# Optimization experiments

Measured on AMD Instinct MI355X. Metric: run time of the kernel, lower is better.

Reference implementation:

```python
import math
import jax, jax.numpy as jnp
import numpy as np

B, T, M, S, D, H = 16, 512, 8, 32, 256, 4
HD = D // H


def setup_inputs() -> dict:
    key = jax.random.key(0)
    ks = jax.random.split(key, 16)
    w = 1.0 / math.sqrt(D)
    return {
        'q_temporal': jax.random.normal(ks[0], (B, T, M, D), jnp.float32),
        'q_static': jax.random.normal(ks[1], (B, S, D), jnp.float32),
        'k_temporal': jax.random.normal(ks[2], (B, T, M, D), jnp.float32),
        'v_temporal': jax.random.normal(ks[3], (B, T, M, D), jnp.float32),
        'k_static': jax.random.normal(ks[4], (B, S, D), jnp.float32),
        'v_static': jax.random.normal(ks[5], (B, S, D), jnp.float32),
        'q_w': jax.random.normal(ks[6], (D, D), jnp.float32) * w,
        'q_b': jax.random.normal(ks[7], (D,), jnp.float32) * w,
        'k_w': jax.random.normal(ks[8], (D, D), jnp.float32) * w,
        'k_b': jax.random.normal(ks[9], (D,), jnp.float32) * w,
        'v_w': jax.random.normal(ks[10], (D, D), jnp.float32) * w,
        'v_b': jax.random.normal(ks[11], (D,), jnp.float32) * w,
        'o_w': jax.random.normal(ks[12], (D, D), jnp.float32) * w,
        'o_b': jax.random.normal(ks[13], (D,), jnp.float32) * w,
        'mask_temporal': jax.random.randint(ks[14], (B, T, M), 0, 2).astype(jnp.int32),
        'mask_fcst': jax.random.randint(ks[15], (B, T, M), 0, 2).astype(jnp.int32),
        'mask_static': jnp.ones((B, S), jnp.int32),
    }


def _lin(x, w, b):
    # torch.nn.Linear: y = x @ W^T + b
    return x @ w.T + b


def reference(q_temporal, q_static, k_temporal, v_temporal, k_static, v_static,
              q_w, q_b, k_w, k_b, v_w, v_b, o_w, o_b,
              mask_temporal, mask_fcst, mask_static):
    scale = 1.0 / math.sqrt(HD)

    def heads5(x):  # [B,T,M,D] -> [B,H,T,M,HD]
        return x.reshape(B, T, M, H, HD).transpose(0, 3, 1, 2, 4)

    def heads3(x):  # [B,S,D] -> [B,H,S,HD]
        return x.reshape(B, -1, H, HD).transpose(0, 2, 1, 3)

    Qt = heads5(_lin(q_temporal, q_w, q_b))
    Kt = heads5(_lin(k_temporal, k_w, k_b))
    Vt = heads5(_lin(v_temporal, v_w, v_b))
    Qs = heads3(_lin(q_static, q_w, q_b))
    Ks = heads3(_lin(k_static, k_w, k_b))
    Vs = heads3(_lin(v_static, v_w, v_b))

    # additive masks: 0 where valid (==1), -inf where padded
    mt = jnp.where(mask_temporal == 1, 0.0, -jnp.inf).astype(Qt.dtype)  # [B,T,M]
    ms = jnp.where(mask_static == 1, 0.0, -jnp.inf).astype(Qt.dtype)    # [B,S]

    # ---- temporal query branch ----
    # temp_temp: per-timestep modality-vs-modality attention, column key mask
    Qt_Kt = jnp.einsum('bhtmd,bhtnd->bhtmn', Qt, Kt) * scale + mt[:, None, :, None, :]
    # temp_static: temporal queries vs static keys
    Qt_Ks = jnp.einsum('bhtmd,bhsd->bhtms', Qt, Ks) * scale + ms[:, None, None, None, :]
    tw = jax.nn.softmax(jnp.concatenate([Qt_Kt, Qt_Ks], axis=-1), axis=-1)  # [B,H,T,M,M+S]
    QKV_t = (jnp.einsum('bhtmn,bhtnd->bhtmd', tw[..., :M], Vt)
             + jnp.einsum('bhtms,bhsd->bhtmd', tw[..., M:], Vs))
    out_t = _lin(QKV_t.transpose(0, 2, 3, 1, 4).reshape(B, T, M, D), o_w, o_b)

    # ---- static query branch ----
    Ktf = Kt.reshape(B, H, T * M, HD)  # flatten (T,M) key axis
    Vtf = Vt.reshape(B, H, T * M, HD)
    Qs_Kt = jnp.einsum('bhqd,bhkd->bhqk', Qs, Ktf) * scale + mt.reshape(B, 1, 1, T * M)
    Qs_Ks = jnp.einsum('bhqd,bhsd->bhqs', Qs, Ks) * scale + ms[:, None, None, :]
    sw = jax.nn.softmax(jnp.concatenate([Qs_Kt, Qs_Ks], axis=-1), axis=-1)  # [B,H,S,T*M+S]
    QKV_s = (jnp.einsum('bhqk,bhkd->bhqd', sw[..., :T * M], Vtf)
             + jnp.einsum('bhqs,bhsd->bhqd', sw[..., T * M:], Vs))
    out_s = _lin(QKV_s.transpose(0, 2, 1, 3).reshape(B, S, D), o_w, o_b)

    return (out_t, out_s, tw, sw)
```

## Files before the change

### kernel.cpp

```cpp
#include <hip/hip_runtime.h>

#define B_   16
#define T_   512
#define M_   8
#define S_   32
#define D_   256
#define H_   4
#define HD_  64
#define TM_  4096
#define NKT  40
#define NKS  4128

typedef unsigned short u16;
typedef __attribute__((ext_vector_type(8))) short bf16x8;
typedef __attribute__((ext_vector_type(4))) float f32x4;

__device__ __forceinline__ u16 f2b(float f) {
    union { float f; unsigned u; } v; v.f = f;
    unsigned r = v.u + 0x7FFF + ((v.u >> 16) & 1);
    return (u16)(r >> 16);
}
__device__ __forceinline__ float blo(unsigned u) {
    union { unsigned i; float f; } v; v.i = u << 16; return v.f;
}
__device__ __forceinline__ float bhi(unsigned u) {
    union { unsigned i; float f; } v; v.i = u & 0xFFFF0000u; return v.f;
}
__device__ __forceinline__ float b2f(u16 u) {
    union { unsigned i; float f; } v; v.i = ((unsigned)u) << 16; return v.f;
}
__device__ __forceinline__ unsigned pack2(float lo, float hi) {
    return (unsigned)f2b(lo) | ((unsigned)f2b(hi) << 16);
}
__device__ __forceinline__ uint4 cvt8(float4 a, float4 b) {
    uint4 r;
    r.x = pack2(a.x, a.y); r.y = pack2(a.z, a.w);
    r.z = pack2(b.x, b.y); r.w = pack2(b.z, b.w);
    return r;
}

#define GLL16(g, l) __builtin_amdgcn_global_load_lds( \
    (const __attribute__((address_space(1))) void*)(g), \
    (__attribute__((address_space(3))) void*)(l), 16, 0, 0)

__global__ __launch_bounds__(256) void k_cvt_w(const float* __restrict__ W0,
                                               const float* __restrict__ W1,
                                               const float* __restrict__ W2,
                                               u16* __restrict__ dst)
{
    const int sel = blockIdx.y;
    const float* W = sel == 0 ? W0 : sel == 1 ? W1 : W2;
    u16* d = dst + sel * 65536;
    const int i0 = (blockIdx.x * 256 + threadIdx.x) * 8;
    const float4 a = *(const float4*)(W + i0);
    const float4 b = *(const float4*)(W + i0 + 4);
    *(uint4*)(d + i0) = cvt8(a, b);
}

template<int XBF, int OUTF32>
__device__ __forceinline__ void gemm_body(const void* __restrict__ Xv,
                                          const u16* __restrict__ Wb,
                                          const float* __restrict__ bias,
                                          void* __restrict__ Yv,
                                          int bx, u16* smem)
{
    const int tid = threadIdx.x;
    const size_t r0 = (size_t)bx * 128;
    const int wave = tid >> 6, lane = tid & 63;
    const int c = lane & 15, g = lane >> 4;
    const int swzk = g ^ ((c >> 1) & 3);
    const int swzl = (lane & 3) ^ ((lane >> 3) & 3);
    u16* sA = smem;
    u16* sB = smem + 10240;
    const int ar = tid >> 1, ah = tid & 1;

    f32x4 acc[8][4];
#pragma unroll
    for (int i = 0; i < 8; ++i)
#pragma unroll
        for (int j = 0; j < 4; ++j) acc[i][j] = (f32x4){0, 0, 0, 0};

    float4 fa[2][4];
    uint4  ua[2][2];

#define LOAD_A(k0, s)                                                           \
    if (XBF) {                                                                  \
        const u16* gA = (const u16*)Xv + (r0 + ar) * 256 + (k0) + ah * 16;      \
        ua[s][0] = *(const uint4*)gA; ua[s][1] = *(const uint4*)(gA + 8);       \
    } else {                                                                    \
        const float* gA = (const float*)Xv + (r0 + ar) * 256 + (k0) + ah * 16;  \
        fa[s][0] = *(const float4*)gA;       fa[s][1] = *(const float4*)(gA + 4); \
        fa[s][2] = *(const float4*)(gA + 8); fa[s][3] = *(const float4*)(gA + 12); \
    }
#define WRITE_A(bi, s)                                                          \
    {   u16* d = sA + (bi) * 5120 + ar * 40 + ah * 16;                          \
        if (XBF) { *(uint4*)d = ua[s][0]; *(uint4*)(d + 8) = ua[s][1]; }        \
        else { *(uint4*)d = cvt8(fa[s][0], fa[s][1]);                           \
               *(uint4*)(d + 8) = cvt8(fa[s][2], fa[s][3]); }                   \
    }
#define STAGE_B(k0, bi)                                                         \
    _Pragma("unroll")                                                           \
    for (int i = 0; i < 4; ++i) {                                               \
        const int row = i * 64 + wave * 16 + (lane >> 2);                       \
        GLL16(Wb + (size_t)row * 256 + (k0) + swzl * 8,                         \
              sB + (bi) * 8192 + (i * 256 + wave * 64) * 8);                    \
    }

    {
        LOAD_A(0, 0)
        WRITE_A(0, 0)
        LOAD_A(32, 0)
        STAGE_B(0, 0)
    }

#pragma unroll
    for (int k = 0; k < 8; ++k) {
        const int cur = k & 1;
        __syncthreads();
        if (k < 6) LOAD_A((k + 2) * 32, (k + 1) & 1)
        if (k < 7) STAGE_B((k + 1) * 32, cur ^ 1)
        bf16x8 a[8], b[4];
#pragma unroll
        for (int f = 0; f < 8; ++f)
            a[f] = *(const bf16x8*)(sA + cur * 5120 + (f * 16 + c) * 40 + g * 8);
#pragma unroll
        for (int f = 0; f < 4; ++f)
            b[f] = *(const bf16x8*)(sB + cur * 8192 + (wave * 64 + f * 16 + c) * 32 + swzk * 8);
#pragma unroll
        for (int rf = 0; rf < 8; ++rf)
#pragma unroll
            for (int cf = 0; cf < 4; ++cf)
                acc[rf][cf] = __builtin_amdgcn_mfma_f32_16x16x32_bf16(
                    a[rf], b[cf], acc[rf][cf], 0, 0, 0);
        if (k < 7) WRITE_A(cur ^ 1, k & 1)
    }
#undef LOAD_A
#undef WRITE_A
#undef STAGE_B

    const int orow = g * 4, ocol = c;
    if (OUTF32) {
#pragma unroll
        for (int cf = 0; cf < 4; ++cf) {
            const int col = wave * 64 + cf * 16 + ocol;
            const float bv = bias[col];
#pragma unroll
            for (int rf = 0; rf < 8; ++rf)
#pragma unroll
                for (int r = 0; r < 4; ++r)
                    ((float*)Yv)[(r0 + rf * 16 + orow + r) * 256 + col] =
                        acc[rf][cf][r] + bv;
        }
    } else {
#pragma unroll
        for (int hh = 0; hh < 2; ++hh) {
            __syncthreads();
#pragma unroll
            for (int cf = 0; cf < 4; ++cf) {
                const int col = wave * 64 + cf * 16 + ocol;
                const float bv = bias[col];
#pragma unroll
                for (int rf4 = 0; rf4 < 4; ++rf4)
#pragma unroll
                    for (int r = 0; r < 4; ++r)
                        smem[(rf4 * 16 + orow + r) * 264 + col] =
                            f2b(acc[hh * 4 + rf4][cf][r] + bv);
            }
            __syncthreads();
#pragma unroll
            for (int i = 0; i < 8; ++i) {
                const int s = i * 256 + tid;
                const int row = s >> 5, seg = s & 31;
                *(uint4*)((u16*)Yv + (r0 + hh * 64 + row) * 256 + seg * 8) =
                    *(const uint4*)(smem + row * 264 + seg * 8);
            }
        }
    }
}

template<int XBF, int OUTF32>
__global__ __launch_bounds__(256, 2) void k_gemm_m(const void* __restrict__ Xv,
                                                   const u16* __restrict__ Wb,
                                                   const float* __restrict__ bias,
                                                   void* __restrict__ Yv)
{
    __shared__ __align__(16) u16 smem[26624];
    gemm_body<XBF, OUTF32>(Xv, Wb, bias, Yv, blockIdx.x, smem);
}

__global__ __launch_bounds__(256, 2) void k_gemm_qkv(
    const float* __restrict__ X0, const float* __restrict__ X1, const float* __restrict__ X2,
    const u16* __restrict__ Wb,
    const float* __restrict__ b0, const float* __restrict__ b1, const float* __restrict__ b2,
    u16* __restrict__ Y0, u16* __restrict__ Y1, u16* __restrict__ Y2)
{
    __shared__ __align__(16) u16 smem[26624];
    const int sel = blockIdx.y;
    const float* X = sel == 0 ? X0 : sel == 1 ? X1 : X2;
    const float* bb = sel == 0 ? b0 : sel == 1 ? b1 : b2;
    u16* Y = sel == 0 ? Y0 : sel == 1 ? Y1 : Y2;
    gemm_body<0, 0>(X, Wb + sel * 65536, bb, Y, blockIdx.x, smem);
}

__global__ __launch_bounds__(256) void k_attn_t(
    const u16* __restrict__ Qt, const u16* __restrict__ Kt, const u16* __restrict__ Vt,
    const u16* __restrict__ Ks, const u16* __restrict__ Vs,
    const int* __restrict__ maskT, const int* __restrict__ maskS,
    float* __restrict__ tw, u16* __restrict__ qkvt)
{
    const int tp = blockIdx.x, b = blockIdx.y;
    const int t0 = tp * 2;
    __shared__ __align__(16) u16 sQ [4 * 2 * 16 * 32];
    __shared__ __align__(16) u16 sKT[4 * 2 * 16 * 32];
    __shared__ __align__(16) u16 sKS[4 * 2 * 32 * 32];
    __shared__ __align__(16) u16 sVT[4 * 64 * 72];
    __shared__ __align__(16) u16 sP [4 * 16 * 72];
    __shared__ int smT[2][8];
    __shared__ int smS[32];
    const int tid = threadIdx.x;

#pragma unroll
    for (int i = 0; i < 2; ++i) {
        const int fl = tid + i * 256;
        const int r = fl >> 5, c32 = fl & 31;
        const int h = c32 >> 3, ks = (c32 >> 2) & 1, seg = c32 & 3;
        const size_t src = (((size_t)b * T_ + t0 + (r >> 3)) * 8 + (r & 7)) * 256 + c32 * 8;
        const int dst = h * 1024 + ks * 512 + r * 32 + seg * 8;
        *(uint4*)(sQ  + dst) = *(const uint4*)(Qt + src);
        *(uint4*)(sKT + dst) = *(const uint4*)(Kt + src);
    }
#pragma unroll
    for (int i = 0; i < 4; ++i) {
        const int fl = tid + i * 256;
        const int r = fl >> 5, c32 = fl & 31;
        const int h = c32 >> 3, ks = (c32 >> 2) & 1, seg = c32 & 3;
        *(uint4*)(sKS + h * 2048 + ks * 1024 + r * 32 + seg * 8) =
            *(const uint4*)(Ks + ((size_t)b * S_ + r) * 256 + c32 * 8);
    }
    {
        const int key = tid & 63, dg = tid >> 6;
        const u16* vrow = nullptr;
        if (key < 16)      vrow = Vt + (((size_t)b * T_ + t0 + (key >> 3)) * 8 + (key & 7)) * 256;
        else if (key < 48) vrow = Vs + ((size_t)b * S_ + (key - 16)) * 256;
#pragma unroll
        for (int i = 0; i < 8; ++i) {
            const int dseg = dg * 8 + i;
            uint4 v = {0, 0, 0, 0};
            if (vrow) v = *(const uint4*)(vrow + dseg * 8);
            const int h = dseg >> 3, dl0 = (dseg & 7) * 8;
            const u16* pv = (const u16*)&v;
#pragma unroll
            for (int j = 0; j < 8; ++j)
                sVT[h * 4608 + (dl0 + j) * 72 + key] = pv[j];
        }
    }
    if (tid < 16) smT[tid >> 3][tid & 7] =
        maskT[((size_t)b * T_ + t0 + (tid >> 3)) * 8 + (tid & 7)];
    if (tid < 32) smS[tid] = maskS[b * S_ + tid];
    __syncthreads();

    const int h = tid >> 6, lane = tid & 63;
    const int c = lane & 15, g = lane >> 4, th = g >> 1;

    f32x4 at = {0,0,0,0}, as0 = {0,0,0,0}, as1 = {0,0,0,0};
#pragma unroll
    for (int ks = 0; ks < 2; ++ks) {
        bf16x8 aq = *(const bf16x8*)(sQ  + h * 1024 + ks * 512 + c * 32 + g * 8);
        bf16x8 bt = *(const bf16x8*)(sKT + h * 1024 + ks * 512 + c * 32 + g * 8);
        bf16x8 b0 = *(const bf16x8*)(sKS + h * 2048 + ks * 1024 + c * 32 + g * 8);
        bf16x8 b1 = *(const bf16x8*)(sKS + h * 2048 + ks * 1024 + 512 + c * 32 + g * 8);
        at  = __builtin_amdgcn_mfma_f32_16x16x32_bf16(aq, bt, at, 0, 0, 0);
        as0 = __builtin_amdgcn_mfma_f32_16x16x32_bf16(aq, b0, as0, 0, 0, 0);
        as1 = __builtin_amdgcn_mfma_f32_16x16x32_bf16(aq, b1, as1, 0, 0, 0);
    }

    const int vt = ((c >> 3) == th) ? smT[th][c & 7] : 0;
    const int v0 = smS[c], v1 = smS[16 + c];
    float st[4], s0[4], s1[4], mx[4];
#pragma unroll
    for (int r = 0; r < 4; ++r) {
        st[r] = vt ? at[r]  * 0.125f : -1e30f;
        s0[r] = v0 ? as0[r] * 0.125f : -1e30f;
        s1[r] = v1 ? as1[r] * 0.125f : -1e30f;
        mx[r] = fmaxf(fmaxf(st[r], s0[r]), s1[r]);
    }
#pragma unroll
    for (int o = 1; o < 16; o <<= 1)
#pragma unroll
        for (int r = 0; r < 4; ++r) mx[r] = fmaxf(mx[r], __shfl_xor(mx[r], o));
    float pt[4], p0[4], p1[4], sum[4];
#pragma unroll
    for (int r = 0; r < 4; ++r) {
        pt[r] = __expf(st[r] - mx[r]);
        p0[r] = __expf(s0[r] - mx[r]);
        p1[r] = __expf(s1[r] - mx[r]);
        sum[r] = pt[r] + p0[r] + p1[r];
    }
#pragma unroll
    for (int o = 1; o < 16; o <<= 1)
#pragma unroll
        for (int r = 0; r < 4; ++r) sum[r] += __shfl_xor(sum[r], o);
#pragma unroll
    for (int r = 0; r < 4; ++r) {
        const float inv = 1.0f / sum[r];
        pt[r] *= inv; p0[r] *= inv; p1[r] *= inv;
    }

#pragma unroll
    for (int r = 0; r < 4; ++r) {
        const int row = g * 4 + r;
        const int tt = t0 + (row >> 3), m = row & 7;
        float* twp = tw + ((((size_t)b * H_ + h) * T_ + tt) * 8 + m) * NKT;
        if ((c >> 3) == th) twp[c & 7] = pt[r];
        twp[8 + c]  = p0[r];
        twp[24 + c] = p1[r];
        u16* sp = sP + h * 1152 + row * 72;
        sp[c]      = f2b(pt[r]);
        sp[16 + c] = f2b(p0[r]);
        sp[32 + c] = f2b(p1[r]);
        sp[48 + c] = 0;
    }

    f32x4 o4[4] = {{0,0,0,0}, {0,0,0,0}, {0,0,0,0}, {0,0,0,0}};
#pragma unroll
    for (int ks = 0; ks < 2; ++ks) {
        bf16x8 pa = *(const bf16x8*)(sP + h * 1152 + c * 72 + ks * 32 + g * 8);
#pragma unroll
        for (int dt = 0; dt < 4; ++dt) {
            bf16x8 pb = *(const bf16x8*)(sVT + h * 4608 + (dt * 16 + c) * 72 + ks * 32 + g * 8);
            o4[dt] = __builtin_amdgcn_mfma_f32_16x16x32_bf16(pa, pb, o4[dt], 0, 0, 0);
        }
    }
#pragma unroll
    for (int dt = 0; dt < 4; ++dt)
#pragma unroll
        for (int r = 0; r < 4; ++r) {
            const int row = g * 4 + r;
            const int tt = t0 + (row >> 3), m = row & 7;
            qkvt[(((size_t)b * T_ + tt) * 8 + m) * 256 + h * 64 + dt * 16 + c] = f2b(o4[dt][r]);
        }
}

__global__ __launch_bounds__(256) void k_attn_s_scores(
    const u16* __restrict__ Qs, const u16* __restrict__ Kt, const u16* __restrict__ Ks,
    const int* __restrict__ maskT, const int* __restrict__ maskS,
    float* __restrict__ raw)
{
    const int ch = blockIdx.x, h = blockIdx.y, b = blockIdx.z;
    const int nk = (ch < 32) ? 128 : 32;
    const int k0 = ch * 128;
    __shared__ __align__(16) u16 sQ[2 * 32 * 32];
    __shared__ __align__(16) u16 sK[2 * 128 * 32];
    __shared__ int sM[128];
    const int tid = threadIdx.x;

    {   const int q = tid >> 3, c8 = tid & 7;
        const int ks = c8 >> 2, seg = c8 & 3;
        *(uint4*)(sQ + ks * 1024 + q * 32 + seg * 8) =
            *(const uint4*)(Qs + ((size_t)b * S_ + q) * 256 + h * 64 + c8 * 8);
    }
#pragma unroll
    for (int i = 0; i < 4; ++i) {
        const int fl = tid + i * 256;
        const int key = fl >> 3, c8 = fl & 7;
        const int ks = c8 >> 2, seg = c8 & 3;
        if (key < nk) {
            const u16* src = (ch < 32)
                ? (Kt + ((size_t)b * TM_ + k0 + key) * 256 + h * 64 + c8 * 8)
                : (Ks + ((size_t)b * S_  +      key) * 256 + h * 64 + c8 * 8);
            *(uint4*)(sK + ks * 4096 + key * 32 + seg * 8) = *(const uint4*)src;
        }
    }
    if (tid < nk) sM[tid] = (ch < 32) ? maskT[(size_t)b * TM_ + k0 + tid]
                                      : maskS[b * S_ + tid];
    __syncthreads();

    const int w = tid >> 6, lane = tid & 63;
    if (w * 32 >= nk) return;
    const int c = lane & 15, g = lane >> 4;

    f32x4 acc[2][2] = {{{0,0,0,0}, {0,0,0,0}}, {{0,0,0,0}, {0,0,0,0}}};
#pragma unroll
    for (int ks = 0; ks < 2; ++ks) {
        bf16x8 a0 = *(const bf16x8*)(sQ + ks * 1024 +        c * 32 + g * 8);
        bf16x8 a1 = *(const bf16x8*)(sQ + ks * 1024 + 512 +  c * 32 + g * 8);
        bf16x8 b0 = *(const bf16x8*)(sK + ks * 4096 + (w * 32 +      c) * 32 + g * 8);
        bf16x8 b1 = *(const bf16x8*)(sK + ks * 4096 + (w * 32 + 16 + c) * 32 + g * 8);
        acc[0][0] = __builtin_amdgcn_mfma_f32_16x16x32_bf16(a0, b0, acc[0][0], 0, 0, 0);
        acc[0][1] = __builtin_amdgcn_mfma_f32_16x16x32_bf16(a0, b1, acc[0][1], 0, 0, 0);
        acc[1][0] = __builtin_amdgcn_mfma_f32_16x16x32_bf16(a1, b0, acc[1][0], 0, 0, 0);
        acc[1][1] = __builtin_amdgcn_mfma_f32_16x16x32_bf16(a1, b1, acc[1][1], 0, 0, 0);
    }
#pragma unroll
    for (int rt = 0; rt < 2; ++rt)
#pragma unroll
        for (int ct = 0; ct < 2; ++ct) {
            const int kl = w * 32 + ct * 16 + c;
            const float madd = sM[kl] ? 0.f : -1e30f;
#pragma unroll
            for (int r = 0; r < 4; ++r) {
                const int q = rt * 16 + g * 4 + r;
                raw[(((size_t)b * H_ + h) * S_ + q) * NKS + k0 + kl] =
                    acc[rt][ct][r] * 0.125f + madd;
            }
        }
}

__global__ __launch_bounds__(256) void k_attn_s_softmax(
    const float* __restrict__ raw, float* __restrict__ sw)
{
    const int q = blockIdx.x, h = blockIdx.y, b = blockIdx.z;
    __shared__ float sRow[NKS];
    __shared__ float red[8];
    const int tid = threadIdx.x;
    const size_t base = (((size_t)b * H_ + h) * S_ + q) * NKS;

    float mx = -1e30f;
    for (int i = tid; i < NKS; i += 256) {
        const float v = raw[base + i];
        sRow[i] = v;
        mx = fmaxf(mx, v);
    }
    for (int o = 32; o; o >>= 1) mx = fmaxf(mx, __shfl_xor(mx, o));
    if ((tid & 63) == 0) red[tid >> 6] = mx;
    __syncthreads();
    mx = fmaxf(fmaxf(red[0], red[1]), fmaxf(red[2], red[3]));

    float sum = 0.f;
    for (int i = tid; i < NKS; i += 256) {
        const float e = __expf(sRow[i] - mx);
        sRow[i] = e;
        sum += e;
    }
    for (int o = 32; o; o >>= 1) sum += __shfl_xor(sum, o);
    if ((tid & 63) == 0) red[4 + (tid >> 6)] = sum;
    __syncthreads();
    sum = (red[4] + red[5]) + (red[6] + red[7]);
    const float inv = 1.0f / sum;

    for (int i = tid; i < NKS; i += 256)
        sw[base + i] = sRow[i] * inv;
}

__global__ __launch_bounds__(256) void k_attn_s_pv_part(
    const float* __restrict__ w, const u16* __restrict__ Vt, const u16* __restrict__ Vs,
    float* __restrict__ part)
{
    const int ch = blockIdx.x, h = blockIdx.y, b = blockIdx.z;
    const int nk = (ch < 32) ? 128 : 32;
    const int k0 = ch * 128;
    __shared__ float sW[32][132];
    __shared__ __align__(16) u16 sV[128 * 64];
    const int tid = threadIdx.x;

#pragma unroll
    for (int i = 0; i < 4; ++i) {
        const int fl = tid + i * 256;
        const int q = fl >> 5, k4 = fl & 31;
        if (k4 * 4 < nk)
            *(float4*)&sW[q][k4 * 4] =
                *(const float4*)(w + (((size_t)b * H_ + h) * S_ + q) * NKS + k0 + k4 * 4);
    }
#pragma unroll
    for (int i = 0; i < 4; ++i) {
        const int fl = tid + i * 256;
        const int key = fl >> 3, pp = fl & 7;
        if (key < nk) {
            const u16* src = (ch < 32)
                ? (Vt + ((size_t)b * TM_ + k0 + key) * D_ + h * HD_ + pp * 8)
                : (Vs + ((size_t)b * S_  +      key) * D_ + h * HD_ + pp * 8);
            ((uint4*)sV)[fl] = *(const uint4*)src;
        }
    }
    __syncthreads();

    const int d = tid & 63, qg = tid >> 6;
    float acc[8] = {0,0,0,0,0,0,0,0};
    for (int kk = 0; kk < nk; kk += 4) {
        const float v0 = b2f(sV[(kk + 0) * 64 + d]);
        const float v1 = b2f(sV[(kk + 1) * 64 + d]);
        const float v2 = b2f(sV[(kk + 2) * 64 + d]);
        const float v3 = b2f(sV[(kk + 3) * 64 + d]);
#pragma unroll
        for (int j = 0; j < 8; ++j) {
            const float4 wv = *(const float4*)&sW[qg * 8 + j][kk];
            acc[j] += wv.x * v0 + wv.y * v1 + wv.z * v2 + wv.w * v3;
        }
    }

    float* pb = part + (((size_t)ch * B_ + b) * H_ + h) * 2048;
#pragma unroll
    for (int j = 0; j < 8; ++j)
        pb[(qg * 8 + j) * 64 + d] = acc[j];
}

__global__ __launch_bounds__(256) void k_attn_s_pv_red(
    const float* __restrict__ part, u16* __restrict__ qkvs)
{
    const int h = blockIdx.x, b = blockIdx.y;
    const int tid = threadIdx.x;
    for (int i = tid; i < 2048; i += 256) {
        float s = 0.f;
#pragma unroll
        for (int c = 0; c < 33; ++c)
            s += part[(((size_t)c * B_ + b) * H_ + h) * 2048 + i];
        const int q = i >> 6, d = i & 63;
        qkvs[((size_t)b * S_ + q) * D_ + h * HD_ + d] = f2b(s);
    }
}

extern "C" void kernel_launch(void* const* d_in, const int* in_sizes, int n_in,
                              void* d_out, int out_size, void* d_ws, size_t ws_size,
                              hipStream_t stream)
{
    const float* q_t = (const float*)d_in[0];
    const float* q_s = (const float*)d_in[1];
    const float* k_t = (const float*)d_in[2];
    const float* v_t = (const float*)d_in[3];
    const float* k_s = (const float*)d_in[4];
    const float* v_s = (const float*)d_in[5];
    const float* q_w = (const float*)d_in[6];
    const float* q_b = (const float*)d_in[7];
    const float* k_w = (const float*)d_in[8];
    const float* k_b = (const float*)d_in[9];
    const float* v_w = (const float*)d_in[10];
    const float* v_b = (const float*)d_in[11];
    const float* o_w = (const float*)d_in[12];
    const float* o_b = (const float*)d_in[13];
    const int* maskT = (const int*)d_in[14];
    const int* maskS = (const int*)d_in[16];
    float* out = (float*)d_out;

    char* ws = (char*)d_ws;
    u16*   Kt   = (u16*)(ws + 0);
    u16*   Vt   = (u16*)(ws + 33554432);
    u16*   QKVt = (u16*)(ws + 67108864);
    float* part = (float*)(ws + 67108864);
    u16*   Wqkv = (u16*)(ws + 67108864);
    u16*   Qs   = (u16*)(ws + 100663296);
    u16*   Ks   = (u16*)(ws + 100925440);
    u16*   Vs   = (u16*)(ws + 101187584);
    u16*   QKVs = (u16*)(ws + 101449728);
    u16*   Qt   = (u16*)(ws + 101711872);
    float* raw  = (float*)(ws + 101711872);
    u16*   Wo   = (u16*)(ws + 101711872);
    if (ws_size < 135528448) return;

    float* out_t = out;
    float* out_s = out + 16777216;
    float* tw    = out + 16908288;
    float* sw    = out + 27394048;

    const dim3 blk(256);
    k_cvt_w<<<dim3(32, 3), blk, 0, stream>>>(q_w, k_w, v_w, Wqkv);

    k_gemm_qkv<<<dim3(512, 3), blk, 0, stream>>>(q_t, k_t, v_t, Wqkv,
                                                 q_b, k_b, v_b, Qt, Kt, Vt);
    k_gemm_qkv<<<dim3(4, 3),   blk, 0, stream>>>(q_s, k_s, v_s, Wqkv,
                                                 q_b, k_b, v_b, Qs, Ks, Vs);

    k_attn_t<<<dim3(256, 16), blk, 0, stream>>>(Qt, Kt, Vt, Ks, Vs, maskT, maskS, tw, QKVt);

    k_cvt_w<<<dim3(32, 1), blk, 0, stream>>>(o_w, o_w, o_w, Wo);
    k_gemm_m<1,1><<<dim3(512), blk, 0, stream>>>(QKVt, Wo, o_b, out_t);

    k_attn_s_scores<<<dim3(33, 4, 16), blk, 0, stream>>>(Qs, Kt, Ks, maskT, maskS, raw);
    k_attn_s_softmax<<<dim3(32, 4, 16), blk, 0, stream>>>(raw, sw);
    k_cvt_w<<<dim3(32, 1), blk, 0, stream>>>(o_w, o_w, o_w, Wo);
    k_attn_s_pv_part<<<dim3(33, 4, 16), blk, 0, stream>>>(sw, Vt, Vs, part);
    k_attn_s_pv_red<<<dim3(4, 16), blk, 0, stream>>>(part, QKVs);

    k_gemm_m<1,1><<<dim3(4),   blk, 0, stream>>>(QKVs, Wo, o_b, out_s);
}
```

Baseline: 267.6 us.

## Rework projection GEMM to 64-row tiles with whole-K A panel preloaded in LDS

Replaces the 128-row tiled GEMM, whose A tile was double-buffered through registers, with a 64-row kernel. That kernel loads the full 64x256 A panel into LDS once (converting fp32 to bf16) and pipelines only the weight tiles. This removes the per-step register staging of A and halves the accumulator count, which should improve occupancy and double the number of blocks. In exchange it puts a large serialized A load up front and reloads the weights twice as often. All four projection GEMM launches are unified into one templated kernel.

```diff
diff --git a/kernel.cpp b/kernel.cpp
--- a/kernel.cpp
+++ b/kernel.cpp
@@ -58,84 +58,82 @@
 }
 
 template<int XBF, int OUTF32>
-__device__ __forceinline__ void gemm_body(const void* __restrict__ Xv,
-                                          const u16* __restrict__ Wb,
-                                          const float* __restrict__ bias,
-                                          void* __restrict__ Yv,
-                                          int bx, u16* smem)
-{
+__global__ __launch_bounds__(256, 2) void k_gemm_db(
+    const void* __restrict__ X0, const void* __restrict__ X1, const void* __restrict__ X2,
+    const u16* __restrict__ Wb, int wstride,
+    const float* __restrict__ b0, const float* __restrict__ b1, const float* __restrict__ b2,
+    void* __restrict__ Y0, void* __restrict__ Y1, void* __restrict__ Y2)
+{
+    __shared__ __align__(16) u16 sA[20480];
+    __shared__ __align__(16) u16 sB[16384];
+    const int sel = blockIdx.y;
+    const void*  Xv   = sel == 0 ? X0 : sel == 1 ? X1 : X2;
+    const float* bias = sel == 0 ? b0 : sel == 1 ? b1 : b2;
+    void*        Yv   = sel == 0 ? Y0 : sel == 1 ? Y1 : Y2;
+    const u16* W = Wb + sel * wstride;
     const int tid = threadIdx.x;
-    const size_t r0 = (size_t)bx * 128;
+    const size_t r0 = (size_t)blockIdx.x * 64;
     const int wave = tid >> 6, lane = tid & 63;
     const int c = lane & 15, g = lane >> 4;
     const int swzk = g ^ ((c >> 1) & 3);
     const int swzl = (lane & 3) ^ ((lane >> 3) & 3);
-    u16* sA = smem;
-    u16* sB = smem + 10240;
-    const int ar = tid >> 1, ah = tid & 1;
-
-    f32x4 acc[8][4];
-#pragma unroll
-    for (int i = 0; i < 8; ++i)
-#pragma unroll
-        for (int j = 0; j < 4; ++j) acc[i][j] = (f32x4){0, 0, 0, 0};
-
-    float4 fa[2][4];
-    uint4  ua[2][2];
-
-#define LOAD_A(k0, s)                                                           \
-    if (XBF) {                                                                  \
-        const u16* gA = (const u16*)Xv + (r0 + ar) * 256 + (k0) + ah * 16;      \
-        ua[s][0] = *(const uint4*)gA; ua[s][1] = *(const uint4*)(gA + 8);       \
-    } else {                                                                    \
-        const float* gA = (const float*)Xv + (r0 + ar) * 256 + (k0) + ah * 16;  \
-        fa[s][0] = *(const float4*)gA;       fa[s][1] = *(const float4*)(gA + 4); \
-        fa[s][2] = *(const float4*)(gA + 8); fa[s][3] = *(const float4*)(gA + 12); \
-    }
-#define WRITE_A(bi, s)                                                          \
-    {   u16* d = sA + (bi) * 5120 + ar * 40 + ah * 16;                          \
-        if (XBF) { *(uint4*)d = ua[s][0]; *(uint4*)(d + 8) = ua[s][1]; }        \
-        else { *(uint4*)d = cvt8(fa[s][0], fa[s][1]);                           \
-               *(uint4*)(d + 8) = cvt8(fa[s][2], fa[s][3]); }                   \
-    }
+
 #define STAGE_B(k0, bi)                                                         \
     _Pragma("unroll")                                                           \
     for (int i = 0; i < 4; ++i) {                                               \
         const int row = i * 64 + wave * 16 + (lane >> 2);                       \
-        GLL16(Wb + (size_t)row * 256 + (k0) + swzl * 8,                         \
+        GLL16(W + (size_t)row * 256 + (k0) + swzl * 8,                          \
               sB + (bi) * 8192 + (i * 256 + wave * 64) * 8);                    \
     }
 
-    {
-        LOAD_A(0, 0)
-        WRITE_A(0, 0)
-        LOAD_A(32, 0)
-        STAGE_B(0, 0)
-    }
+    STAGE_B(0, 0)
+
+    if (XBF) {
+#pragma unroll
+        for (int j = 0; j < 8; ++j) {
+            const int row = j * 8 + wave * 2 + (lane >> 5);
+            const uint4 v = *(const uint4*)((const u16*)Xv + (r0 + row) * 256
+                                            + (lane & 31) * 8);
+            *(uint4*)(sA + ((lane & 31) >> 2) * 2560 + row * 40 + (lane & 3) * 8) = v;
+        }
+    } else {
+#pragma unroll
+        for (int j = 0; j < 16; ++j) {
+            const int row = j * 4 + wave;
+            const float4 v = *(const float4*)((const float*)Xv + (r0 + row) * 256
+                                              + lane * 4);
+            uint2 p; p.x = pack2(v.x, v.y); p.y = pack2(v.z, v.w);
+            *(uint2*)(sA + (lane >> 3) * 2560 + row * 40 + (lane & 7) * 4) = p;
+        }
+    }
+    __syncthreads();
+
+    f32x4 acc[4][4];
+#pragma unroll
+    for (int i = 0; i < 4; ++i)
+#pragma unroll
+        for (int j = 0; j < 4; ++j) acc[i][j] = (f32x4){0, 0, 0, 0};
 
 #pragma unroll
     for (int k = 0; k < 8; ++k) {
         const int cur = k & 1;
-        __syncthreads();
-        if (k < 6) LOAD_A((k + 2) * 32, (k + 1) & 1)
-        if (k < 7) STAGE_B((k + 1) * 32, cur ^ 1)
-        bf16x8 a[8], b[4];
-#pragma unroll
-        for (int f = 0; f < 8; ++f)
-            a[f] = *(const bf16x8*)(sA + cur * 5120 + (f * 16 + c) * 40 + g * 8);
+        if (k < 7) { STAGE_B((k + 1) * 32, cur ^ 1) }
+        bf16x8 a[4], b[4];
 #pragma unroll
         for (int f = 0; f < 4; ++f)
-            b[f] = *(const bf16x8*)(sB + cur * 8192 + (wave * 64 + f * 16 + c) * 32 + swzk * 8);
-#pragma unroll
-        for (int rf = 0; rf < 8; ++rf)
+            a[f] = *(const bf16x8*)(sA + k * 2560 + (f * 16 + c) * 40 + g * 8);
+#pragma unroll
+        for (int f = 0; f < 4; ++f)
+            b[f] = *(const bf16x8*)(sB + cur * 8192
+                                    + (wave * 64 + f * 16 + c) * 32 + swzk * 8);
+#pragma unroll
+        for (int rf = 0; rf < 4; ++rf)
 #pragma unroll
             for (int cf = 0; cf < 4; ++cf)
                 acc[rf][cf] = __builtin_amdgcn_mfma_f32_16x16x32_bf16(
                     a[rf], b[cf], acc[rf][cf], 0, 0, 0);
-        if (k < 7) WRITE_A(cur ^ 1, k & 1)
-    }
-#undef LOAD_A
-#undef WRITE_A
+        if (k < 7) __syncthreads();
+    }
 #undef STAGE_B
 
     const int orow = g * 4, ocol = c;
@@ -145,61 +143,33 @@
             const int col = wave * 64 + cf * 16 + ocol;
             const float bv = bias[col];
 #pragma unroll
-            for (int rf = 0; rf < 8; ++rf)
+            for (int rf = 0; rf < 4; ++rf)
 #pragma unroll
                 for (int r = 0; r < 4; ++r)
                     ((float*)Yv)[(r0 + rf * 16 + orow + r) * 256 + col] =
                         acc[rf][cf][r] + bv;
         }
     } else {
-#pragma unroll
-        for (int hh = 0; hh < 2; ++hh) {
-            __syncthreads();
-#pragma unroll
-            for (int cf = 0; cf < 4; ++cf) {
-                const int col = wave * 64 + cf * 16 + ocol;
-                const float bv = bias[col];
-#pragma unroll
-                for (int rf4 = 0; rf4 < 4; ++rf4)
-#pragma unroll
-                    for (int r = 0; r < 4; ++r)
-                        smem[(rf4 * 16 + orow + r) * 264 + col] =
-                            f2b(acc[hh * 4 + rf4][cf][r] + bv);
-            }
-            __syncthreads();
-#pragma unroll
-            for (int i = 0; i < 8; ++i) {
-                const int s = i * 256 + tid;
-                const int row = s >> 5, seg = s & 31;
-                *(uint4*)((u16*)Yv + (r0 + hh * 64 + row) * 256 + seg * 8) =
-                    *(const uint4*)(smem + row * 264 + seg * 8);
-            }
-        }
-    }
-}
-
-template<int XBF, int OUTF32>
-__global__ __launch_bounds__(256, 2) void k_gemm_m(const void* __restrict__ Xv,
-                                                   const u16* __restrict__ Wb,
-                                                   const float* __restrict__ bias,
-                                                   void* __restrict__ Yv)
-{
-    __shared__ __align__(16) u16 smem[26624];
-    gemm_body<XBF, OUTF32>(Xv, Wb, bias, Yv, blockIdx.x, smem);
-}
-
-__global__ __launch_bounds__(256, 2) void k_gemm_qkv(
-    const float* __restrict__ X0, const float* __restrict__ X1, const float* __restrict__ X2,
-    const u16* __restrict__ Wb,
-    const float* __restrict__ b0, const float* __restrict__ b1, const float* __restrict__ b2,
-    u16* __restrict__ Y0, u16* __restrict__ Y1, u16* __restrict__ Y2)
-{
-    __shared__ __align__(16) u16 smem[26624];
-    const int sel = blockIdx.y;
-    const float* X = sel == 0 ? X0 : sel == 1 ? X1 : X2;
-    const float* bb = sel == 0 ? b0 : sel == 1 ? b1 : b2;
-    u16* Y = sel == 0 ? Y0 : sel == 1 ? Y1 : Y2;
-    gemm_body<0, 0>(X, Wb + sel * 65536, bb, Y, blockIdx.x, smem);
+        __syncthreads();
+#pragma unroll
+        for (int cf = 0; cf < 4; ++cf) {
+            const int col = wave * 64 + cf * 16 + ocol;
+            const float bv = bias[col];
+#pragma unroll
+            for (int rf = 0; rf < 4; ++rf)
+#pragma unroll
+                for (int r = 0; r < 4; ++r)
+                    sA[(rf * 16 + orow + r) * 264 + col] = f2b(acc[rf][cf][r] + bv);
+        }
+        __syncthreads();
+#pragma unroll
+        for (int i = 0; i < 8; ++i) {
+            const int s = i * 256 + tid;
+            const int row = s >> 5, seg = s & 31;
+            *(uint4*)((u16*)Yv + (r0 + row) * 256 + seg * 8) =
+                *(const uint4*)(sA + row * 264 + seg * 8);
+        }
+    }
 }
 
 __global__ __launch_bounds__(256) void k_attn_t(
@@ -554,15 +524,16 @@
     const dim3 blk(256);
     k_cvt_w<<<dim3(32, 3), blk, 0, stream>>>(q_w, k_w, v_w, Wqkv);
 
-    k_gemm_qkv<<<dim3(512, 3), blk, 0, stream>>>(q_t, k_t, v_t, Wqkv,
-                                                 q_b, k_b, v_b, Qt, Kt, Vt);
-    k_gemm_qkv<<<dim3(4, 3),   blk, 0, stream>>>(q_s, k_s, v_s, Wqkv,
-                                                 q_b, k_b, v_b, Qs, Ks, Vs);
+    k_gemm_db<0, 0><<<dim3(1024, 3), blk, 0, stream>>>(
+        q_t, k_t, v_t, Wqkv, 65536, q_b, k_b, v_b, Qt, Kt, Vt);
+    k_gemm_db<0, 0><<<dim3(8, 3), blk, 0, stream>>>(
+        q_s, k_s, v_s, Wqkv, 65536, q_b, k_b, v_b, Qs, Ks, Vs);
 
     k_attn_t<<<dim3(256, 16), blk, 0, stream>>>(Qt, Kt, Vt, Ks, Vs, maskT, maskS, tw, QKVt);
 
     k_cvt_w<<<dim3(32, 1), blk, 0, stream>>>(o_w, o_w, o_w, Wo);
-    k_gemm_m<1,1><<<dim3(512), blk, 0, stream>>>(QKVt, Wo, o_b, out_t);
+    k_gemm_db<1, 1><<<dim3(1024, 1), blk, 0, stream>>>(
+        QKVt, QKVt, QKVt, Wo, 0, o_b, o_b, o_b, out_t, out_t, out_t);
 
     k_attn_s_scores<<<dim3(33, 4, 16), blk, 0, stream>>>(Qs, Kt, Ks, maskT, maskS, raw);
     k_attn_s_softmax<<<dim3(32, 4, 16), blk, 0, stream>>>(raw, sw);
@@ -570,5 +541,6 @@
     k_attn_s_pv_part<<<dim3(33, 4, 16), blk, 0, stream>>>(sw, Vt, Vs, part);
     k_attn_s_pv_red<<<dim3(4, 16), blk, 0, stream>>>(part, QKVs);
 
-    k_gemm_m<1,1><<<dim3(4),   blk, 0, stream>>>(QKVs, Wo, o_b, out_s);
-}
+    k_gemm_db<1, 1><<<dim3(8, 1), blk, 0, stream>>>(
+        QKVs, QKVs, QKVs, Wo, 0, o_b, o_b, o_b, out_s, out_s, out_s);
+}
```

Result: no change. 263.3 us (-1.6%).
